# Optimization experiments

Hardware: AMD Instinct MI355X
Metric: run time of the kernel (lower is better)

The kernel has to match this reference:

```python
import jax, jax.numpy as jnp
import numpy as np

N = 256   # n_nodes == input_dim (table columns)
B = 1024  # batch size
D = 64    # decoder_dim / encoder_dim


def setup_inputs() -> dict:
    key = jax.random.key(0)
    ks = jax.random.split(key, 10)
    r = lambda k, sh, s=0.05: jax.random.normal(k, sh, dtype=jnp.float32) * s
    return {
        "x": jax.random.normal(ks[0], (B, N), dtype=jnp.float32),
        "eps": jax.random.normal(ks[1], (B, N), dtype=jnp.float32),
        "graph_logits": r(ks[2], (N, N), 0.5),
        "W_enc": r(ks[3], (N, D)),
        "b_enc": jnp.zeros((D,), jnp.float32),
        "W_mu": r(ks[4], (D, N)),
        "b_mu": jnp.zeros((N,), jnp.float32),
        "W_lv": r(ks[5], (D, N)),
        "b_lv": jnp.zeros((N,), jnp.float32),
        "emb_W": r(ks[6], (N, N + 1, D)),   # per-column Linear(input_dim+1 -> decoder_dim)
        "emb_b": jnp.zeros((N, D), jnp.float32),
        "gc1_W": r(ks[7], (D, D // 2)),
        "gc1_b": jnp.zeros((D // 2,), jnp.float32),
        "gc2_W": r(ks[8], (D // 2, 1)),
        "gc2_b": jnp.zeros((1,), jnp.float32),
        "it_num": 10,
    }


def _graph_conv(h, adj, W, b):
    # DGL GraphConv(norm='both', weight, bias) with edge_weight = adj values.
    # Edges go row->col of adj; degrees are unweighted nonzero counts.
    dt = h.dtype
    deg_out = jnp.sum(adj != 0, axis=1).astype(dt)  # out-degree of source node
    deg_in = jnp.sum(adj != 0, axis=0).astype(dt)   # in-degree of destination node
    norm_src = deg_out ** -0.5
    norm_dst = deg_in ** -0.5
    h = h * norm_src[None, :, None]                 # scale source features
    agg = jnp.einsum('bnd,nm->bmd', h, adj)         # sum_i adj[i,j] * h[:, i]
    agg = agg * norm_dst[None, :, None]
    return agg @ W + b


def reference(x, eps, graph_logits, W_enc, b_enc, W_mu, b_mu, W_lv, b_lv,
              emb_W, emb_b, gc1_W, gc1_b, gc2_W, gc2_b, it_num):
    # --- Encoder (MLP-VAE, encoder_l=2 => single Linear+ReLU trunk) ---
    h = jax.nn.relu(x @ W_enc + b_enc)
    mu = h @ W_mu + b_mu
    logvar = h @ W_lv + b_lv
    z = mu + eps * jnp.exp(0.5 * logvar)            # reparameterize, (B, N)
    # --- LearnedGraph ---
    g = jax.nn.sigmoid(graph_logits)
    eye = jnp.eye(N, dtype=g.dtype)
    adj = g * (1.0 - eye) + eye                      # force self-loops to 1
    if it_num > 50:                                  # nn.Threshold(threshold, 0)
        adj = jnp.where(adj > 0.1, adj, 0.0)
    # --- GraphInputProcessorHomo: het encoding + per-column embeddings ---
    b_z = jnp.concatenate(
        [z[:, :, None], jnp.broadcast_to(eye, (z.shape[0], N, N))], axis=-1
    )                                                # (B, N, N+1)
    b_z = jnp.tanh(jnp.einsum('bnf,nfd->bnd', b_z, emb_W) + emb_b[None])  # (B, N, D)
    # --- GraphDecoderHomo ('gcn'): GraphConv(64->32, tanh) -> GraphConv(32->1) ---
    h1 = jnp.tanh(_graph_conv(b_z, adj, gc1_W, gc1_b))
    h2 = _graph_conv(h1, adj, gc2_W, gc2_b)          # (B, N, 1)
    x_hat = h2.reshape(z.shape[0], -1)               # (B, N)
    return x_hat
```

## Files before the change

### kernel.cpp

```cpp
#include <hip/hip_runtime.h>
#include <hip/hip_bf16.h>
#include <math.h>

#define NN 256
#define BB 1024
#define DD 64

typedef short bf16x8 __attribute__((ext_vector_type(8)));
typedef float f32x4 __attribute__((ext_vector_type(4)));

__device__ __forceinline__ float ftanh(float x) {
    float e = __expf(2.0f * x);
    return 1.0f - 2.0f * __builtin_amdgcn_rcpf(e + 1.0f);
}

__device__ __forceinline__ unsigned short f2bf(float v) {
    __hip_bfloat16 h = __float2bfloat16(v);
    return *reinterpret_cast<unsigned short*>(&h);
}

__device__ __forceinline__ float bf2f(unsigned short u) {
    union { unsigned int i; float f; } c;
    c.i = ((unsigned int)u) << 16;
    return c.f;
}

__global__ __launch_bounds__(256) void k1_enc(
    const float* __restrict__ x, const float* __restrict__ Wenc,
    const float* __restrict__ benc, float* __restrict__ H)
{
    int t = threadIdx.x;
    int d = t & 63;
    int b = (blockIdx.x << 2) + (t >> 6);
    const float* xr = x + b * NN;
    float acc = benc[d];
    for (int n = 0; n < NN; n += 4) {
        float4 xv = *(const float4*)&xr[n];
        acc = fmaf(xv.x, Wenc[(n + 0) * DD + d], acc);
        acc = fmaf(xv.y, Wenc[(n + 1) * DD + d], acc);
        acc = fmaf(xv.z, Wenc[(n + 2) * DD + d], acc);
        acc = fmaf(xv.w, Wenc[(n + 3) * DD + d], acc);
    }
    H[b * DD + d] = fmaxf(acc, 0.0f);
}

__global__ __launch_bounds__(256) void k2_z(
    const float* __restrict__ H, const float* __restrict__ Wmu,
    const float* __restrict__ bmu, const float* __restrict__ Wlv,
    const float* __restrict__ blv, const float* __restrict__ eps,
    float* __restrict__ ZT)
{
    __shared__ float Hs[4][DD];
    int t = threadIdx.x;
    int b0 = blockIdx.x << 2;
    Hs[t >> 6][t & 63] = H[((b0 + (t >> 6)) << 6) + (t & 63)];
    __syncthreads();
    int n = t;
    float mu[4], lv[4];
    float bm = bmu[n], bl = blv[n];
#pragma unroll
    for (int i = 0; i < 4; ++i) { mu[i] = bm; lv[i] = bl; }
    for (int d = 0; d < DD; ++d) {
        float wm = Wmu[d * NN + n];
        float wl = Wlv[d * NN + n];
#pragma unroll
        for (int i = 0; i < 4; ++i) {
            float h = Hs[i][d];
            mu[i] = fmaf(h, wm, mu[i]);
            lv[i] = fmaf(h, wl, lv[i]);
        }
    }
#pragma unroll
    for (int i = 0; i < 4; ++i) {
        int b = b0 + i;
        float z = fmaf(eps[b * NN + n], expf(0.5f * lv[i]), mu[i]);
        ZT[n * BB + b] = z;
    }
}

__global__ __launch_bounds__(256) void k3a(
    const float* __restrict__ gl, const int* __restrict__ itp,
    float* __restrict__ adj, float* __restrict__ dego)
{
    int nrow = blockIdx.x, m = threadIdx.x;
    float v = gl[nrow * NN + m];
    float a = (nrow == m) ? 1.0f : 1.0f / (1.0f + expf(-v));
    if (itp[0] > 50 && !(a > 0.1f)) a = 0.0f;
    adj[nrow * NN + m] = a;
    unsigned long long ball = __ballot(a != 0.0f);
    __shared__ int cnt_s[4];
    if ((m & 63) == 0) cnt_s[m >> 6] = __popcll(ball);
    __syncthreads();
    if (m == 0) dego[nrow] = (float)(cnt_s[0] + cnt_s[1] + cnt_s[2] + cnt_s[3]);
}

__global__ __launch_bounds__(256) void k3b(
    const float* __restrict__ adj, const float* __restrict__ dego,
    float* __restrict__ adjw, unsigned short* __restrict__ adjwt)
{
    int m = blockIdx.x, nrow = threadIdx.x;
    float a = adj[nrow * NN + m];
    unsigned long long ball = __ballot(a != 0.0f);
    __shared__ int cnt_s[4];
    __shared__ float din_s;
    if ((nrow & 63) == 0) cnt_s[nrow >> 6] = __popcll(ball);
    __syncthreads();
    if (nrow == 0) din_s = (float)(cnt_s[0] + cnt_s[1] + cnt_s[2] + cnt_s[3]);
    __syncthreads();
    float w = a * (1.0f / sqrtf(dego[nrow])) * (1.0f / sqrtf(din_s));
    adjw[nrow * NN + m] = w;
    adjwt[m * NN + nrow] = f2bf(w);
}

__global__ __launch_bounds__(256) void k4_mfma(
    const float* __restrict__ ZT, const float* __restrict__ embW,
    const float* __restrict__ embB, const float* __restrict__ g1W,
    unsigned short* __restrict__ P1TT)
{
    __shared__ float As[8][64], Cs[8][64], zs[8][64];
    __shared__ float Ws[32][68];
    __shared__ unsigned short Dst[64][32][8];
    int t = threadIdx.x;
    int w = t >> 6, l = t & 63;
    int lo = l & 15, q = l >> 4;
    int q8 = q << 3;
    int nb = blockIdx.x & 31, bb = blockIdx.x >> 5;
    int n0 = nb << 3, b0 = bb << 6;

    for (int i = t; i < 512; i += 256) {
        int ni = i >> 6, d = i & 63;
        size_t eb = (size_t)(n0 + ni) * (257 * 64);
        As[ni][d] = embW[eb + d];
        Cs[ni][d] = embW[eb + ((size_t)(n0 + ni + 1) << 6) + d]
                  + embB[((n0 + ni) << 6) + d];
        zs[ni][d] = ZT[(size_t)(n0 + ni) * BB + b0 + d];
    }
    for (int i = t; i < 2048; i += 256) {
        int d = i >> 5, k = i & 31;
        Ws[k][d] = g1W[i];
    }
    __syncthreads();

    bf16x8 bwh[2][2], bwl[2][2];
#pragma unroll
    for (int nt = 0; nt < 2; ++nt)
#pragma unroll
        for (int kc = 0; kc < 2; ++kc) {
            float4 w0 = *(const float4*)&Ws[(nt << 4) + lo][(kc << 5) + q8];
            float4 w1 = *(const float4*)&Ws[(nt << 4) + lo][(kc << 5) + q8 + 4];
            float v[8] = {w0.x, w0.y, w0.z, w0.w, w1.x, w1.y, w1.z, w1.w};
            bf16x8 h, lq;
#pragma unroll
            for (int j = 0; j < 8; ++j) {
                unsigned short hb = f2bf(v[j]);
                h[j] = (short)hb;
                lq[j] = (short)f2bf(v[j] - bf2f(hb));
            }
            bwh[nt][kc] = h;
            bwl[nt][kc] = lq;
        }

    for (int ni = 0; ni < 8; ++ni) {
        float zv = zs[ni][(w << 4) + lo];
        f32x4 acc0 = (f32x4)0.0f, acc1 = (f32x4)0.0f;
#pragma unroll
        for (int kc = 0; kc < 2; ++kc) {
            float4 a0 = *(const float4*)&As[ni][(kc << 5) + q8];
            float4 a1 = *(const float4*)&As[ni][(kc << 5) + q8 + 4];
            float4 c0 = *(const float4*)&Cs[ni][(kc << 5) + q8];
            float4 c1 = *(const float4*)&Cs[ni][(kc << 5) + q8 + 4];
            float e[8];
            e[0] = ftanh(fmaf(zv, a0.x, c0.x));
            e[1] = ftanh(fmaf(zv, a0.y, c0.y));
            e[2] = ftanh(fmaf(zv, a0.z, c0.z));
            e[3] = ftanh(fmaf(zv, a0.w, c0.w));
            e[4] = ftanh(fmaf(zv, a1.x, c1.x));
            e[5] = ftanh(fmaf(zv, a1.y, c1.y));
            e[6] = ftanh(fmaf(zv, a1.z, c1.z));
            e[7] = ftanh(fmaf(zv, a1.w, c1.w));
            bf16x8 ehi, elo;
#pragma unroll
            for (int j = 0; j < 8; ++j) {
                unsigned short hb = f2bf(e[j]);
                ehi[j] = (short)hb;
                elo[j] = (short)f2bf(e[j] - bf2f(hb));
            }
            acc0 = __builtin_amdgcn_mfma_f32_16x16x32_bf16(ehi, bwh[0][kc], acc0, 0, 0, 0);
            acc0 = __builtin_amdgcn_mfma_f32_16x16x32_bf16(elo, bwh[0][kc], acc0, 0, 0, 0);
            acc0 = __builtin_amdgcn_mfma_f32_16x16x32_bf16(ehi, bwl[0][kc], acc0, 0, 0, 0);
            acc1 = __builtin_amdgcn_mfma_f32_16x16x32_bf16(ehi, bwh[1][kc], acc1, 0, 0, 0);
            acc1 = __builtin_amdgcn_mfma_f32_16x16x32_bf16(elo, bwh[1][kc], acc1, 0, 0, 0);
            acc1 = __builtin_amdgcn_mfma_f32_16x16x32_bf16(ehi, bwl[1][kc], acc1, 0, 0, 0);
        }
        int bl = (w << 4) + (q << 2);
#pragma unroll
        for (int r = 0; r < 4; ++r) {
            Dst[bl + r][lo][ni]      = f2bf(acc0[r]);
            Dst[bl + r][16 + lo][ni] = f2bf(acc1[r]);
        }
    }
    __syncthreads();

    const uint4* dsp = (const uint4*)&Dst[0][0][0];
    size_t obase = ((size_t)b0 * 32) * NN + n0;
#pragma unroll
    for (int i = 0; i < 8; ++i) {
        int p = (i << 8) + t;
        uint4 v = dsp[p];
        *(uint4*)&P1TT[obase + (size_t)p * NN] = v;
    }
}

__global__ __launch_bounds__(256) void k5_mfma(
    const unsigned short* __restrict__ adjwt, const unsigned short* __restrict__ p1tt,
    const float* __restrict__ g1b, const float* __restrict__ g2w,
    float* __restrict__ Q)
{
    int t = threadIdx.x;
    int w = t >> 6, l = t & 63;
    int c = l & 15, q = l >> 4;
    int j0 = blockIdx.x << 6;
    int mbase = w << 6;

    f32x4 acc[4][4];
#pragma unroll
    for (int i = 0; i < 4; ++i)
#pragma unroll
        for (int j = 0; j < 4; ++j) acc[i][j] = (f32x4)0.0f;

    const unsigned short* ap[4];
    const unsigned short* bp[4];
#pragma unroll
    for (int mi = 0; mi < 4; ++mi)
        ap[mi] = adjwt + (size_t)(mbase + (mi << 4) + c) * NN + (q << 3);
#pragma unroll
    for (int ji = 0; ji < 4; ++ji)
        bp[ji] = p1tt + (size_t)(j0 + (ji << 4) + c) * NN + (q << 3);

#pragma unroll 2
    for (int n0 = 0; n0 < NN; n0 += 32) {
        bf16x8 af[4], bf[4];
#pragma unroll
        for (int mi = 0; mi < 4; ++mi) af[mi] = *(const bf16x8*)(ap[mi] + n0);
#pragma unroll
        for (int ji = 0; ji < 4; ++ji) bf[ji] = *(const bf16x8*)(bp[ji] + n0);
#pragma unroll
        for (int mi = 0; mi < 4; ++mi)
#pragma unroll
            for (int ji = 0; ji < 4; ++ji)
                acc[mi][ji] = __builtin_amdgcn_mfma_f32_16x16x32_bf16(
                    af[mi], bf[ji], acc[mi][ji], 0, 0, 0);
    }

    float b1v0 = g1b[c],      g2v0 = g2w[c];
    float b1v1 = g1b[16 + c], g2v1 = g2w[16 + c];
    int bb0 = blockIdx.x << 1;
#pragma unroll
    for (int mi = 0; mi < 4; ++mi) {
#pragma unroll
        for (int bb = 0; bb < 2; ++bb) {
            float red[4];
#pragma unroll
            for (int r = 0; r < 4; ++r) {
                float s = ftanh(acc[mi][(bb << 1) + 0][r] + b1v0) * g2v0
                        + ftanh(acc[mi][(bb << 1) + 1][r] + b1v1) * g2v1;
                s += __shfl_xor(s, 1);
                s += __shfl_xor(s, 2);
                s += __shfl_xor(s, 4);
                s += __shfl_xor(s, 8);
                red[r] = s;
            }
            float* qp = &Q[(size_t)(bb0 + bb) * NN + mbase + (mi << 4) + (q << 2)];
            if (c == 0) qp[0] = red[0];
            if (c == 1) qp[1] = red[1];
            if (c == 2) qp[2] = red[2];
            if (c == 3) qp[3] = red[3];
        }
    }
}

__global__ __launch_bounds__(256) void k6_gc2(
    const float* __restrict__ Q, const float* __restrict__ adjw,
    const float* __restrict__ g2b, float* __restrict__ xh)
{
    __shared__ float At[64][17];
    __shared__ __align__(16) float Bt[16][64];
    int t = threadIdx.x;
    int tx = t & 15, ty = t >> 4;
    int mt = blockIdx.x & 3, bt = blockIdx.x >> 2;
    int m0 = mt << 6, b0 = bt << 6;
    float acc[4][4];
#pragma unroll
    for (int i = 0; i < 4; ++i)
#pragma unroll
        for (int j = 0; j < 4; ++j) acc[i][j] = 0.0f;

    for (int kb = 0; kb < NN; kb += 16) {
        for (int i = t; i < 1024; i += 256) {
            int kk = i & 15, c = i >> 4;
            At[c][kk] = Q[(b0 + c) * NN + kb + kk];
        }
        for (int i = t; i < 1024; i += 256) {
            int mj = i & 63, kk = i >> 6;
            Bt[kk][mj] = adjw[(kb + kk) * NN + m0 + mj];
        }
        __syncthreads();
#pragma unroll
        for (int kk = 0; kk < 16; ++kk) {
            float4 bq = *(const float4*)&Bt[kk][tx << 2];
            float am[4];
#pragma unroll
            for (int bi = 0; bi < 4; ++bi) am[bi] = At[(ty << 2) + bi][kk];
#pragma unroll
            for (int bi = 0; bi < 4; ++bi) {
                acc[bi][0] = fmaf(am[bi], bq.x, acc[bi][0]);
                acc[bi][1] = fmaf(am[bi], bq.y, acc[bi][1]);
                acc[bi][2] = fmaf(am[bi], bq.z, acc[bi][2]);
                acc[bi][3] = fmaf(am[bi], bq.w, acc[bi][3]);
            }
        }
        __syncthreads();
    }
    float bias = g2b[0];
#pragma unroll
    for (int bi = 0; bi < 4; ++bi) {
        float4 v = make_float4(acc[bi][0] + bias, acc[bi][1] + bias,
                               acc[bi][2] + bias, acc[bi][3] + bias);
        *(float4*)&xh[(b0 + (ty << 2) + bi) * NN + m0 + (tx << 2)] = v;
    }
}

extern "C" void kernel_launch(void* const* d_in, const int* in_sizes, int n_in,
                              void* d_out, int out_size, void* d_ws, size_t ws_size,
                              hipStream_t stream) {
    const float* x    = (const float*)d_in[0];
    const float* eps  = (const float*)d_in[1];
    const float* gl   = (const float*)d_in[2];
    const float* Wenc = (const float*)d_in[3];
    const float* benc = (const float*)d_in[4];
    const float* Wmu  = (const float*)d_in[5];
    const float* bmu  = (const float*)d_in[6];
    const float* Wlv  = (const float*)d_in[7];
    const float* blv  = (const float*)d_in[8];
    const float* embW = (const float*)d_in[9];
    const float* embB = (const float*)d_in[10];
    const float* g1W  = (const float*)d_in[11];
    const float* g1b  = (const float*)d_in[12];
    const float* g2W  = (const float*)d_in[13];
    const float* g2b  = (const float*)d_in[14];
    const int*   itp  = (const int*)d_in[15];

    float* ws   = (float*)d_ws;
    float* H    = ws;
    float* ZT   = ws + 65536;
    float* ADJR = ws + 327680;
    float* DEGO = ws + 393216;
    float* ADJW = ws + 393472;
    unsigned short* ADJWT = (unsigned short*)(ws + 459008);
    unsigned short* P1TT  = (unsigned short*)(ws + 491776);
    float* Qb   = ws + 4686080;
    float* xh   = (float*)d_out;

    k1_enc  <<<256, 256, 0, stream>>>(x, Wenc, benc, H);
    k2_z    <<<256, 256, 0, stream>>>(H, Wmu, bmu, Wlv, blv, eps, ZT);
    k3a     <<<256, 256, 0, stream>>>(gl, itp, ADJR, DEGO);
    k3b     <<<256, 256, 0, stream>>>(ADJR, DEGO, ADJW, ADJWT);
    k4_mfma <<<512, 256, 0, stream>>>(ZT, embW, embB, g1W, P1TT);
    k5_mfma <<<512, 256, 0, stream>>>(ADJWT, P1TT, g1b, g2W, Qb);
    k6_gc2  <<<64,  256, 0, stream>>>(Qb, ADJW, g2b, xh);
}
```

Measured before the change: 205.0 us.

## Fuse encoder kernels and shrink tiles in k4/k5/k6 for more blocks

```diff
diff --git a/kernel.cpp b/kernel.cpp
--- a/kernel.cpp
+++ b/kernel.cpp
@@ -25,27 +25,9 @@
     return c.f;
 }
 
-__global__ __launch_bounds__(256) void k1_enc(
+__global__ __launch_bounds__(256) void k12(
     const float* __restrict__ x, const float* __restrict__ Wenc,
-    const float* __restrict__ benc, float* __restrict__ H)
-{
-    int t = threadIdx.x;
-    int d = t & 63;
-    int b = (blockIdx.x << 2) + (t >> 6);
-    const float* xr = x + b * NN;
-    float acc = benc[d];
-    for (int n = 0; n < NN; n += 4) {
-        float4 xv = *(const float4*)&xr[n];
-        acc = fmaf(xv.x, Wenc[(n + 0) * DD + d], acc);
-        acc = fmaf(xv.y, Wenc[(n + 1) * DD + d], acc);
-        acc = fmaf(xv.z, Wenc[(n + 2) * DD + d], acc);
-        acc = fmaf(xv.w, Wenc[(n + 3) * DD + d], acc);
-    }
-    H[b * DD + d] = fmaxf(acc, 0.0f);
-}
-
-__global__ __launch_bounds__(256) void k2_z(
-    const float* __restrict__ H, const float* __restrict__ Wmu,
+    const float* __restrict__ benc, const float* __restrict__ Wmu,
     const float* __restrict__ bmu, const float* __restrict__ Wlv,
     const float* __restrict__ blv, const float* __restrict__ eps,
     float* __restrict__ ZT)
@@ -53,28 +35,41 @@
     __shared__ float Hs[4][DD];
     int t = threadIdx.x;
     int b0 = blockIdx.x << 2;
-    Hs[t >> 6][t & 63] = H[((b0 + (t >> 6)) << 6) + (t & 63)];
-    __syncthreads();
-    int n = t;
-    float mu[4], lv[4];
-    float bm = bmu[n], bl = blv[n];
-#pragma unroll
-    for (int i = 0; i < 4; ++i) { mu[i] = bm; lv[i] = bl; }
-    for (int d = 0; d < DD; ++d) {
-        float wm = Wmu[d * NN + n];
-        float wl = Wlv[d * NN + n];
+    {
+        int d = t & 63, bl = t >> 6;
+        const float* xr = x + (b0 + bl) * NN;
+        float acc = benc[d];
+        for (int n = 0; n < NN; n += 4) {
+            float4 xv = *(const float4*)&xr[n];
+            acc = fmaf(xv.x, Wenc[(n + 0) * DD + d], acc);
+            acc = fmaf(xv.y, Wenc[(n + 1) * DD + d], acc);
+            acc = fmaf(xv.z, Wenc[(n + 2) * DD + d], acc);
+            acc = fmaf(xv.w, Wenc[(n + 3) * DD + d], acc);
+        }
+        Hs[bl][d] = fmaxf(acc, 0.0f);
+    }
+    __syncthreads();
+    {
+        int n = t;
+        float mu[4], lv[4];
+        float bm = bmu[n], bl_ = blv[n];
+#pragma unroll
+        for (int i = 0; i < 4; ++i) { mu[i] = bm; lv[i] = bl_; }
+        for (int d = 0; d < DD; ++d) {
+            float wm = Wmu[d * NN + n];
+            float wl = Wlv[d * NN + n];
+#pragma unroll
+            for (int i = 0; i < 4; ++i) {
+                float h = Hs[i][d];
+                mu[i] = fmaf(h, wm, mu[i]);
+                lv[i] = fmaf(h, wl, lv[i]);
+            }
+        }
 #pragma unroll
         for (int i = 0; i < 4; ++i) {
-            float h = Hs[i][d];
-            mu[i] = fmaf(h, wm, mu[i]);
-            lv[i] = fmaf(h, wl, lv[i]);
-        }
-    }
-#pragma unroll
-    for (int i = 0; i < 4; ++i) {
-        int b = b0 + i;
-        float z = fmaf(eps[b * NN + n], expf(0.5f * lv[i]), mu[i]);
-        ZT[n * BB + b] = z;
+            int b = b0 + i;
+            ZT[n * BB + b] = fmaf(eps[b * NN + n], expf(0.5f * lv[i]), mu[i]);
+        }
     }
 }
 
@@ -117,18 +112,18 @@
     const float* __restrict__ embB, const float* __restrict__ g1W,
     unsigned short* __restrict__ P1TT)
 {
-    __shared__ float As[8][64], Cs[8][64], zs[8][64];
+    __shared__ float As[4][64], Cs[4][64], zs[4][64];
     __shared__ float Ws[32][68];
-    __shared__ unsigned short Dst[64][32][8];
+    __shared__ __align__(16) unsigned short Dst[64][32][4];
     int t = threadIdx.x;
     int w = t >> 6, l = t & 63;
     int lo = l & 15, q = l >> 4;
     int q8 = q << 3;
-    int nb = blockIdx.x & 31, bb = blockIdx.x >> 5;
-    int n0 = nb << 3, b0 = bb << 6;
-
-    for (int i = t; i < 512; i += 256) {
-        int ni = i >> 6, d = i & 63;
+    int nb = blockIdx.x & 63, bb = blockIdx.x >> 6;
+    int n0 = nb << 2, b0 = bb << 6;
+
+    {
+        int ni = t >> 6, d = t & 63;
         size_t eb = (size_t)(n0 + ni) * (257 * 64);
         As[ni][d] = embW[eb + d];
         Cs[ni][d] = embW[eb + ((size_t)(n0 + ni + 1) << 6) + d]
@@ -160,7 +155,8 @@
             bwl[nt][kc] = lq;
         }
 
-    for (int ni = 0; ni < 8; ++ni) {
+#pragma unroll
+    for (int ni = 0; ni < 4; ++ni) {
         float zv = zs[ni][(w << 4) + lo];
         f32x4 acc0 = (f32x4)0.0f, acc1 = (f32x4)0.0f;
 #pragma unroll
@@ -201,13 +197,13 @@
     }
     __syncthreads();
 
-    const uint4* dsp = (const uint4*)&Dst[0][0][0];
+    const uint2* dsp = (const uint2*)&Dst[0][0][0];
     size_t obase = ((size_t)b0 * 32) * NN + n0;
 #pragma unroll
     for (int i = 0; i < 8; ++i) {
         int p = (i << 8) + t;
-        uint4 v = dsp[p];
-        *(uint4*)&P1TT[obase + (size_t)p * NN] = v;
+        uint2 v = dsp[p];
+        *(uint2*)&P1TT[obase + (size_t)p * NN] = v;
     }
 }
 
@@ -219,19 +215,20 @@
     int t = threadIdx.x;
     int w = t >> 6, l = t & 63;
     int c = l & 15, q = l >> 4;
-    int j0 = blockIdx.x << 6;
-    int mbase = w << 6;
-
-    f32x4 acc[4][4];
-#pragma unroll
-    for (int i = 0; i < 4; ++i)
+    int jt = blockIdx.x >> 1, mh = blockIdx.x & 1;
+    int j0 = jt << 6;
+    int mbase = (mh << 7) + (w << 5);
+
+    f32x4 acc[2][4];
+#pragma unroll
+    for (int i = 0; i < 2; ++i)
 #pragma unroll
         for (int j = 0; j < 4; ++j) acc[i][j] = (f32x4)0.0f;
 
-    const unsigned short* ap[4];
+    const unsigned short* ap[2];
     const unsigned short* bp[4];
 #pragma unroll
-    for (int mi = 0; mi < 4; ++mi)
+    for (int mi = 0; mi < 2; ++mi)
         ap[mi] = adjwt + (size_t)(mbase + (mi << 4) + c) * NN + (q << 3);
 #pragma unroll
     for (int ji = 0; ji < 4; ++ji)
@@ -239,13 +236,13 @@
 
 #pragma unroll 2
     for (int n0 = 0; n0 < NN; n0 += 32) {
-        bf16x8 af[4], bf[4];
-#pragma unroll
-        for (int mi = 0; mi < 4; ++mi) af[mi] = *(const bf16x8*)(ap[mi] + n0);
+        bf16x8 af[2], bf[4];
+#pragma unroll
+        for (int mi = 0; mi < 2; ++mi) af[mi] = *(const bf16x8*)(ap[mi] + n0);
 #pragma unroll
         for (int ji = 0; ji < 4; ++ji) bf[ji] = *(const bf16x8*)(bp[ji] + n0);
 #pragma unroll
-        for (int mi = 0; mi < 4; ++mi)
+        for (int mi = 0; mi < 2; ++mi)
 #pragma unroll
             for (int ji = 0; ji < 4; ++ji)
                 acc[mi][ji] = __builtin_amdgcn_mfma_f32_16x16x32_bf16(
@@ -254,9 +251,9 @@
 
     float b1v0 = g1b[c],      g2v0 = g2w[c];
     float b1v1 = g1b[16 + c], g2v1 = g2w[16 + c];
-    int bb0 = blockIdx.x << 1;
-#pragma unroll
-    for (int mi = 0; mi < 4; ++mi) {
+    int bb0 = jt << 1;
+#pragma unroll
+    for (int mi = 0; mi < 2; ++mi) {
 #pragma unroll
         for (int bb = 0; bb < 2; ++bb) {
             float red[4];
@@ -283,50 +280,37 @@
     const float* __restrict__ Q, const float* __restrict__ adjw,
     const float* __restrict__ g2b, float* __restrict__ xh)
 {
-    __shared__ float At[64][17];
-    __shared__ __align__(16) float Bt[16][64];
+    __shared__ float At[32][33];
+    __shared__ float Bt[32][33];
     int t = threadIdx.x;
     int tx = t & 15, ty = t >> 4;
-    int mt = blockIdx.x & 3, bt = blockIdx.x >> 2;
-    int m0 = mt << 6, b0 = bt << 6;
-    float acc[4][4];
-#pragma unroll
-    for (int i = 0; i < 4; ++i)
-#pragma unroll
-        for (int j = 0; j < 4; ++j) acc[i][j] = 0.0f;
-
-    for (int kb = 0; kb < NN; kb += 16) {
+    int mt = blockIdx.x & 7, bt = blockIdx.x >> 3;
+    int m0 = mt << 5, b0 = bt << 5;
+    float acc[2][2] = {{0.0f, 0.0f}, {0.0f, 0.0f}};
+
+    for (int kb = 0; kb < NN; kb += 32) {
         for (int i = t; i < 1024; i += 256) {
-            int kk = i & 15, c = i >> 4;
-            At[c][kk] = Q[(b0 + c) * NN + kb + kk];
-        }
-        for (int i = t; i < 1024; i += 256) {
-            int mj = i & 63, kk = i >> 6;
-            Bt[kk][mj] = adjw[(kb + kk) * NN + m0 + mj];
+            int r = i >> 5, cc = i & 31;
+            At[r][cc] = Q[(b0 + r) * NN + kb + cc];
+            Bt[r][cc] = adjw[(kb + r) * NN + m0 + cc];
         }
         __syncthreads();
-#pragma unroll
-        for (int kk = 0; kk < 16; ++kk) {
-            float4 bq = *(const float4*)&Bt[kk][tx << 2];
-            float am[4];
-#pragma unroll
-            for (int bi = 0; bi < 4; ++bi) am[bi] = At[(ty << 2) + bi][kk];
-#pragma unroll
-            for (int bi = 0; bi < 4; ++bi) {
-                acc[bi][0] = fmaf(am[bi], bq.x, acc[bi][0]);
-                acc[bi][1] = fmaf(am[bi], bq.y, acc[bi][1]);
-                acc[bi][2] = fmaf(am[bi], bq.z, acc[bi][2]);
-                acc[bi][3] = fmaf(am[bi], bq.w, acc[bi][3]);
-            }
+#pragma unroll 8
+        for (int kk = 0; kk < 32; ++kk) {
+            float bv0 = Bt[kk][tx << 1], bv1 = Bt[kk][(tx << 1) + 1];
+            float a0 = At[ty << 1][kk], a1 = At[(ty << 1) + 1][kk];
+            acc[0][0] = fmaf(a0, bv0, acc[0][0]);
+            acc[0][1] = fmaf(a0, bv1, acc[0][1]);
+            acc[1][0] = fmaf(a1, bv0, acc[1][0]);
+            acc[1][1] = fmaf(a1, bv1, acc[1][1]);
         }
         __syncthreads();
     }
     float bias = g2b[0];
 #pragma unroll
-    for (int bi = 0; bi < 4; ++bi) {
-        float4 v = make_float4(acc[bi][0] + bias, acc[bi][1] + bias,
-                               acc[bi][2] + bias, acc[bi][3] + bias);
-        *(float4*)&xh[(b0 + (ty << 2) + bi) * NN + m0 + (tx << 2)] = v;
+    for (int i = 0; i < 2; ++i) {
+        float2 v = make_float2(acc[i][0] + bias, acc[i][1] + bias);
+        *(float2*)&xh[(b0 + (ty << 1) + i) * NN + m0 + (tx << 1)] = v;
     }
 }
 
@@ -351,7 +335,6 @@
     const int*   itp  = (const int*)d_in[15];
 
     float* ws   = (float*)d_ws;
-    float* H    = ws;
     float* ZT   = ws + 65536;
     float* ADJR = ws + 327680;
     float* DEGO = ws + 393216;
@@ -361,11 +344,10 @@
     float* Qb   = ws + 4686080;
     float* xh   = (float*)d_out;
 
-    k1_enc  <<<256, 256, 0, stream>>>(x, Wenc, benc, H);
-    k2_z    <<<256, 256, 0, stream>>>(H, Wmu, bmu, Wlv, blv, eps, ZT);
-    k3a     <<<256, 256, 0, stream>>>(gl, itp, ADJR, DEGO);
-    k3b     <<<256, 256, 0, stream>>>(ADJR, DEGO, ADJW, ADJWT);
-    k4_mfma <<<512, 256, 0, stream>>>(ZT, embW, embB, g1W, P1TT);
-    k5_mfma <<<512, 256, 0, stream>>>(ADJWT, P1TT, g1b, g2W, Qb);
-    k6_gc2  <<<64,  256, 0, stream>>>(Qb, ADJW, g2b, xh);
-}
+    k12     <<<256,  256, 0, stream>>>(x, Wenc, benc, Wmu, bmu, Wlv, blv, eps, ZT);
+    k3a     <<<256,  256, 0, stream>>>(gl, itp, ADJR, DEGO);
+    k3b     <<<256,  256, 0, stream>>>(ADJR, DEGO, ADJW, ADJWT);
+    k4_mfma <<<1024, 256, 0, stream>>>(ZT, embW, embB, g1W, P1TT);
+    k5_mfma <<<1024, 256, 0, stream>>>(ADJWT, P1TT, g1b, g2W, Qb);
+    k6_gc2  <<<256,  256, 0, stream>>>(Qb, ADJW, g2b, xh);
+}
```

Measured after the change: 180.5 us. 1.14x faster.
